# Performance work log

Measured on AMD Instinct MI355X. Metric: run time of the kernel, lower is better.

## Reference

```python
import jax, jax.numpy as jnp
import numpy as np
from itertools import combinations, product

HID = 32
HEADS = 4
HEAD_DIM = 2


def _e8_roots():
    # 240 E8 roots: 112 of form (+-1,+-1,0^6) permuted, 128 of form (+-1/2)^8 with even # of minus signs
    roots = []
    for i, j in combinations(range(8), 2):
        for si in (1.0, -1.0):
            for sj in (1.0, -1.0):
                v = np.zeros(8); v[i] = si; v[j] = sj
                roots.append(v)
    for signs in product((0.5, -0.5), repeat=8):
        if sum(1 for s in signs if s < 0) % 2 == 0:
            roots.append(np.array(signs))
    return jnp.asarray(np.stack(roots), dtype=jnp.float32)  # [240, 8]


def _nearest_d8(x):
    # nearest point of D8 lattice (integer coords, even coordinate sum)
    f = jnp.round(x)
    err = x - f
    idx = jnp.argmax(jnp.abs(err), axis=-1)  # coord with worst rounding error
    oh = jax.nn.one_hot(idx, 8, dtype=x.dtype)
    e_at = jnp.take_along_axis(err, idx[..., None], axis=-1)  # [B,1]
    g = f + oh * jnp.where(e_at >= 0, 1.0, -1.0)  # flip worst coord the other way
    parity_ok = jnp.mod(f.sum(-1), 2.0) == 0
    return jnp.where(parity_ok[..., None], f, g)


def _nearest_e8(x):
    # E8 = D8  U  (D8 + 1/2)
    y0 = _nearest_d8(x)
    y1 = _nearest_d8(x - 0.5) + 0.5
    d0 = ((x - y0) ** 2).sum(-1, keepdims=True)
    d1 = ((x - y1) ** 2).sum(-1, keepdims=True)
    return jnp.where(d0 <= d1, y0, y1)


def _norm(x, eps=1e-12):
    return x / jnp.maximum(jnp.linalg.norm(x, axis=-1, keepdims=True), eps)


def setup_inputs() -> dict:
    key = jax.random.key(0)
    ks = jax.random.split(key, 16)
    B, N = 524288, 7
    s8, s32 = 1.0 / np.sqrt(8.0), 1.0 / np.sqrt(32.0)
    return {
        'colony_outputs': jax.random.normal(ks[0], (B, N, 8), jnp.float32),
        'colony_confidences': jax.random.uniform(ks[1], (B, N), jnp.float32),
        'Wq': jax.random.uniform(ks[2], (HID, 8), jnp.float32, -s8, s8),
        'bq': jnp.zeros((HID,), jnp.float32),
        'Wk': jax.random.uniform(ks[3], (HID, 8), jnp.float32, -s8, s8),
        'bk': jnp.zeros((HID,), jnp.float32),
        'Wv': jax.random.uniform(ks[4], (8, 8), jnp.float32, -s8, s8),
        'bv': jnp.zeros((8,), jnp.float32),
        'comm': jnp.eye(N, dtype=jnp.float32) + 0.1 * jax.random.normal(ks[5], (N, N), jnp.float32),
        'role': jnp.ones((N,), jnp.float32) + 0.1 * jax.random.normal(ks[6], (N,), jnp.float32),
        'mha_in_w': jax.random.uniform(ks[7], (24, 8), jnp.float32, -s8, s8),
        'mha_in_b': jnp.zeros((24,), jnp.float32),
        'W1': jax.random.uniform(ks[8], (HID, 8), jnp.float32, -s8, s8),
        'b1': jnp.zeros((HID,), jnp.float32),
        'W2': jax.random.uniform(ks[9], (8, HID), jnp.float32, -s32, s32),
        'b2': jnp.zeros((8,), jnp.float32),
        'gate': jnp.asarray(0.1, jnp.float32),
    }


def reference(colony_outputs, colony_confidences, Wq, bq, Wk, bk, Wv, bv,
              comm, role, mha_in_w, mha_in_b, W1, b1, W2, b2, gate):
    roots = _e8_roots()  # [240, 8]
    x = _norm(colony_outputs)  # [B, N, 8] on S^7
    B, N, _ = x.shape

    # --- attention-based colony weights ---
    q = x.mean(axis=1) @ Wq.T + bq                 # [B, HID]
    k = x @ Wk.T + bk                              # [B, N, HID]
    scores = jnp.einsum('bh,bnh->bn', q, k) / np.sqrt(float(HID))
    scores = jnp.einsum('bn,nm->bm', scores, jax.nn.softmax(comm, axis=-1))
    scores = scores + jax.nn.softmax(role)[None, :]

    # multi-head attention weights (embed 8, 4 heads, head_dim 2); dropout off (eval)
    Wq3, Wk3 = mha_in_w[:8], mha_in_w[8:16]
    bq3, bk3 = mha_in_b[:8], mha_in_b[8:16]
    Q = (x @ Wq3.T + bq3).reshape(B, N, HEADS, HEAD_DIM)
    K = (x @ Wk3.T + bk3).reshape(B, N, HEADS, HEAD_DIM)
    A = jax.nn.softmax(jnp.einsum('bnhd,bmhd->bhnm', Q, K) / np.sqrt(float(HEAD_DIM)), axis=-1)
    mhs = A.mean(axis=1).mean(axis=1)              # avg heads -> [B,N,N], mean over queries -> [B,N]
    scores = 0.7 * scores + 0.3 * mhs
    weights = jax.nn.softmax(scores, axis=-1)      # [B, N]

    # confidence modulation
    weights = weights * colony_confidences
    weights = weights / jnp.clip(weights.sum(-1, keepdims=True), 1e-8, None)

    # combine + gated MLP refine
    values = x @ Wv.T + bv                         # [B, N, 8]
    combined = jnp.einsum('bn,bnd->bd', weights, values)  # [B, 8]
    h = jax.nn.gelu(combined @ W1.T + b1, approximate=False) @ W2.T + b2
    refined = _norm(combined + jax.nn.sigmoid(gate) * h)

    # E8 quantization with straight-through estimator (training path)
    hard = _nearest_e8(refined)
    quantized = refined + jax.lax.stop_gradient(hard - refined)
    sq = (refined ** 2).sum(-1, keepdims=True) - 2.0 * refined @ roots.T + (roots ** 2).sum(-1)[None, :]
    indices = jnp.argmin(sq, axis=-1)              # [B]
    return quantized, indices, weights
```

## Files before the change

### kernel.cpp

```cpp
#include <hip/hip_runtime.h>
#include <math.h>

#define INV_SQRT2 0.70710678118654752f
#define INV_SQRT32 0.17677669529663689f

__device__ __forceinline__ void nearest_d8(const float* xx, float* y) {
  float f[8], err[8];
#pragma unroll
  for (int d = 0; d < 8; ++d) { f[d] = rintf(xx[d]); err[d] = xx[d] - f[d]; }
  int idx = 0; float best = -1.0f;
#pragma unroll
  for (int d = 0; d < 8; ++d) { float a = fabsf(err[d]); if (a > best) { best = a; idx = d; } }
  float fs = 0.f;
#pragma unroll
  for (int d = 0; d < 8; ++d) fs += f[d];
  bool ok = ((((int)fs) & 1) == 0);
#pragma unroll
  for (int d = 0; d < 8; ++d) {
    float g = f[d] + ((d == idx) ? ((err[d] >= 0.f) ? 1.f : -1.f) : 0.f);
    y[d] = ok ? f[d] : g;
  }
}

__device__ __forceinline__ float pair_sum(float mine, int half) {
  float o = __shfl_xor(mine, 1, 64);
  return half ? (o + mine) : (mine + o);
}

extern "C" __global__ void __launch_bounds__(256)
e8_kernel(const float* __restrict__ colony, const float* __restrict__ conf,
          const float* __restrict__ Wq, const float* __restrict__ bq,
          const float* __restrict__ Wk, const float* __restrict__ bk,
          const float* __restrict__ Wv, const float* __restrict__ bv,
          const float* __restrict__ comm, const float* __restrict__ role,
          const float* __restrict__ mha_w, const float* __restrict__ mha_b,
          const float* __restrict__ W1, const float* __restrict__ b1,
          const float* __restrict__ W2, const float* __restrict__ b2,
          const float* __restrict__ gate, float* __restrict__ out, int B)
{
  __shared__ float x_lds[56 * 128];
  __shared__ float wlds[7 * 128];
  __shared__ float sM8[64], sU[8], sV[8], sCc[1];
  __shared__ float sComm[49], sRole[7];
  __shared__ float sWq3[64], sWk3[64], sBq3[8], sBk3[8];
  __shared__ float sWv[64], sBv[8];
  __shared__ float sW1[256], sB1[32], sW2[256], sB2[8];
  __shared__ float sGate[1];

  const int t = threadIdx.x;
  if (t < 64) {
    int i = t >> 3, j = t & 7;
    float a = 0.f;
    for (int h = 0; h < 32; ++h) a += Wq[h * 8 + i] * Wk[h * 8 + j];
    sM8[t] = a;
    sWq3[t] = mha_w[t];
    sWk3[t] = mha_w[64 + t];
    sWv[t] = Wv[t];
  } else if (t < 72) {
    int j = t - 64;
    float a = 0.f, bb = 0.f;
    for (int h = 0; h < 32; ++h) { a += bq[h] * Wk[h * 8 + j]; bb += bk[h] * Wq[h * 8 + j]; }
    sU[j] = a; sV[j] = bb;
    sBq3[j] = mha_b[j]; sBk3[j] = mha_b[8 + j]; sBv[j] = bv[j]; sB2[j] = b2[j];
  } else if (t == 72) {
    float c = 0.f;
    for (int h = 0; h < 32; ++h) c += bq[h] * bk[h];
    sCc[0] = c;
    sGate[0] = 1.f / (1.f + expf(-gate[0]));
  } else if (t >= 80 && t < 87) {
    int n = t - 80;
    float mx = -1e30f;
    for (int m = 0; m < 7; ++m) mx = fmaxf(mx, comm[n * 7 + m]);
    float ee[7], s = 0.f;
    for (int m = 0; m < 7; ++m) { ee[m] = expf(comm[n * 7 + m] - mx); s += ee[m]; }
    for (int m = 0; m < 7; ++m) sComm[n * 7 + m] = ee[m] / s;
  } else if (t == 87) {
    float mx = -1e30f;
    for (int m = 0; m < 7; ++m) mx = fmaxf(mx, role[m]);
    float ee[7], s = 0.f;
    for (int m = 0; m < 7; ++m) { ee[m] = expf(role[m] - mx); s += ee[m]; }
    for (int m = 0; m < 7; ++m) sRole[m] = ee[m] / s;
  }
  sW1[t] = W1[t];
  sW2[t] = W2[t];
  if (t < 32) sB1[t] = b1[t];

  const int eloc = t >> 1;
  const int half = t & 1;
  const int el = blockIdx.x * 128 + eloc;
  const int ec = (el < B) ? el : (B - 1);

  {
    const float* px = colony + (size_t)ec * 56;
#pragma unroll
    for (int nn = 0; nn < 4; ++nn) {
      int n = half * 4 + nn;
      if (n < 7) {
        float4 v0 = *(const float4*)(px + n * 8);
        float4 v1 = *(const float4*)(px + n * 8 + 4);
        float row[8] = { v0.x, v0.y, v0.z, v0.w, v1.x, v1.y, v1.z, v1.w };
        float ss = 0.f;
#pragma unroll
        for (int d = 0; d < 8; ++d) ss += row[d] * row[d];
        float inv = 1.0f / fmaxf(sqrtf(ss), 1e-12f);
#pragma unroll
        for (int d = 0; d < 8; ++d) x_lds[(n * 8 + d) * 128 + eloc] = row[d] * inv;
      }
    }
  }
  __syncthreads();

#define LDX(n, j) x_lds[(((n) << 3) + (j)) * 128 + eloc]

  float xm[8];
#pragma unroll
  for (int d = 0; d < 8; ++d) xm[d] = 0.f;
#pragma unroll
  for (int n = 0; n < 7; ++n) {
#pragma unroll
    for (int d = 0; d < 8; ++d) xm[d] += LDX(n, d);
  }
#pragma unroll
  for (int d = 0; d < 8; ++d) xm[d] *= (1.0f / 7.0f);

  float w8[8];
#pragma unroll
  for (int j = 0; j < 8; ++j) {
    float a = 0.f;
#pragma unroll
    for (int i = 0; i < 8; ++i) a += xm[i] * sM8[i * 8 + j];
    w8[j] = a + sU[j];
  }
  float base = sCc[0];
#pragma unroll
  for (int i = 0; i < 8; ++i) base += sV[i] * xm[i];
  float sc[7];
#pragma unroll
  for (int n = 0; n < 7; ++n) {
    float a = base;
#pragma unroll
    for (int j = 0; j < 8; ++j) a += w8[j] * LDX(n, j);
    sc[n] = a * INV_SQRT32;
  }
  float sc2[7];
#pragma unroll
  for (int m = 0; m < 7; ++m) {
    float a = 0.f;
#pragma unroll
    for (int n = 0; n < 7; ++n) a += sc[n] * sComm[n * 7 + m];
    sc2[m] = a + sRole[m];
  }

  float mhs_p[7];
#pragma unroll
  for (int m = 0; m < 7; ++m) mhs_p[m] = 0.f;
#pragma unroll
  for (int hh = 0; hh < 2; ++hh) {
    int h = half * 2 + hh;
    float Kh[7][2], Qh[7][2];
#pragma unroll
    for (int m = 0; m < 7; ++m) {
      float row[8];
#pragma unroll
      for (int j = 0; j < 8; ++j) row[j] = LDX(m, j);
      float k0 = sBk3[2 * h], k1 = sBk3[2 * h + 1];
      float q0 = sBq3[2 * h], q1 = sBq3[2 * h + 1];
#pragma unroll
      for (int j = 0; j < 8; ++j) {
        k0 += row[j] * sWk3[(2 * h) * 8 + j];
        k1 += row[j] * sWk3[(2 * h + 1) * 8 + j];
        q0 += row[j] * sWq3[(2 * h) * 8 + j];
        q1 += row[j] * sWq3[(2 * h + 1) * 8 + j];
      }
      Kh[m][0] = k0; Kh[m][1] = k1;
      Qh[m][0] = q0; Qh[m][1] = q1;
    }
#pragma unroll
    for (int n = 0; n < 7; ++n) {
      float ex[7], mx = -1e30f;
#pragma unroll
      for (int m = 0; m < 7; ++m) {
        float a = Qh[n][0] * Kh[m][0] + Qh[n][1] * Kh[m][1];
        ex[m] = a * INV_SQRT2;
        mx = fmaxf(mx, ex[m]);
      }
      float s = 0.f;
#pragma unroll
      for (int m = 0; m < 7; ++m) { ex[m] = __expf(ex[m] - mx); s += ex[m]; }
      float inv = 1.0f / s;
#pragma unroll
      for (int m = 0; m < 7; ++m) mhs_p[m] += ex[m] * inv;
    }
  }
  float mhs[7];
#pragma unroll
  for (int m = 0; m < 7; ++m) mhs[m] = pair_sum(mhs_p[m], half);

  float scf[7], mx2 = -1e30f;
#pragma unroll
  for (int m = 0; m < 7; ++m) {
    scf[m] = 0.7f * sc2[m] + 0.3f * ((mhs[m] * 0.25f) * (1.0f / 7.0f));
    mx2 = fmaxf(mx2, scf[m]);
  }
  float ew[7], s2 = 0.f;
#pragma unroll
  for (int m = 0; m < 7; ++m) { ew[m] = __expf(scf[m] - mx2); s2 += ew[m]; }
  float sinv = 1.0f / s2;
  float w[7], ws = 0.f;
  const float* pc = conf + (size_t)ec * 7;
#pragma unroll
  for (int m = 0; m < 7; ++m) { w[m] = (ew[m] * sinv) * pc[m]; ws += w[m]; }
  float dinv = 1.0f / fmaxf(ws, 1e-8f);
#pragma unroll
  for (int m = 0; m < 7; ++m) w[m] = w[m] * dinv;

  if (!half) {
#pragma unroll
    for (int m = 0; m < 7; ++m) wlds[eloc * 7 + m] = w[m];
  }

  float xc[8];
#pragma unroll
  for (int d = 0; d < 8; ++d) xc[d] = 0.f;
#pragma unroll
  for (int n = 0; n < 7; ++n) {
#pragma unroll
    for (int d = 0; d < 8; ++d) xc[d] += w[n] * LDX(n, d);
  }
  float comb[8];
#pragma unroll
  for (int i = 0; i < 8; ++i) {
    float a = sBv[i];
#pragma unroll
    for (int j = 0; j < 8; ++j) a += sWv[i * 8 + j] * xc[j];
    comb[i] = a;
  }

  float o8p[8];
#pragma unroll
  for (int k = 0; k < 8; ++k) o8p[k] = half ? 0.f : sB2[k];
#pragma unroll
  for (int ii = 0; ii < 16; ++ii) {
    int i = half * 16 + ii;
    float a = sB1[i];
#pragma unroll
    for (int j = 0; j < 8; ++j) a += sW1[i * 8 + j] * comb[j];
    float g = 0.5f * a * (1.f + erff(a * INV_SQRT2));
#pragma unroll
    for (int k = 0; k < 8; ++k) o8p[k] += sW2[k * 32 + i] * g;
  }
  float o8[8];
#pragma unroll
  for (int k = 0; k < 8; ++k) o8[k] = pair_sum(o8p[k], half);

  float gsig = sGate[0];
  float pre[8], ss2 = 0.f;
#pragma unroll
  for (int d = 0; d < 8; ++d) { pre[d] = comb[d] + gsig * o8[d]; ss2 += pre[d] * pre[d]; }
  float ninv = 1.0f / fmaxf(sqrtf(ss2), 1e-12f);
  float r[8];
#pragma unroll
  for (int d = 0; d < 8; ++d) r[d] = pre[d] * ninv;

  float* outq = out;
  float* outi = out + (size_t)B * 8;
  float* outw = out + (size_t)B * 9;

  {
    float xs[8], y[8];
#pragma unroll
    for (int d = 0; d < 8; ++d) xs[d] = half ? (r[d] - 0.5f) : r[d];
    nearest_d8(xs, y);
#pragma unroll
    for (int d = 0; d < 8; ++d) y[d] = half ? (y[d] + 0.5f) : y[d];
    float dow = 0.f;
#pragma unroll
    for (int d = 0; d < 8; ++d) { float dd = r[d] - y[d]; dow += dd * dd; }
    float doth = __shfl_xor(dow, 1, 64);
    float dd0 = half ? doth : dow;
    float dd1 = half ? dow : doth;
    bool use0 = (dd0 <= dd1);
    bool mine_wins = (use0 == (half == 0));
    if (mine_wins && el < B) {
      float q0v[8];
#pragma unroll
      for (int d = 0; d < 8; ++d) q0v[d] = r[d] + (y[d] - r[d]);
      *(float4*)(outq + (size_t)el * 8)     = make_float4(q0v[0], q0v[1], q0v[2], q0v[3]);
      *(float4*)(outq + (size_t)el * 8 + 4) = make_float4(q0v[4], q0v[5], q0v[6], q0v[7]);
    }
  }

  float ssum = 0.f;
#pragma unroll
  for (int d = 0; d < 8; ++d) ssum += r[d] * r[d];
  float bestSq = 1e30f;
  int bestIdx = 0;
  {
    int idx = 0;
#pragma unroll
    for (int i = 0; i < 8; ++i) {
#pragma unroll
      for (int j = i + 1; j < 8; ++j) {
        float a = r[i] + r[j];
        float bb = r[i] - r[j];
        float c0 = half ? -bb : a;
        float c1 = half ? -a : bb;
        float sq0 = fmaf(-2.f, c0, ssum) + 2.f;
        if (sq0 < bestSq) { bestSq = sq0; bestIdx = idx + 2 * half; }
        float sq1 = fmaf(-2.f, c1, ssum) + 2.f;
        if (sq1 < bestSq) { bestSq = sq1; bestIdx = idx + 2 * half + 1; }
        idx += 4;
      }
    }
  }
  {
    float hr[8];
#pragma unroll
    for (int d = 0; d < 8; ++d) hr[d] = 0.5f * r[d];
    float sumhr = ((hr[0] + hr[1]) + (hr[2] + hr[3])) + ((hr[4] + hr[5]) + (hr[6] + hr[7]));
    float Thi[16], Tlo[16];
#pragma unroll
    for (int m = 0; m < 16; ++m) {
      float s1 = 0.f, sB_ = 0.f;
      if (m & 8) { s1 += hr[0]; sB_ += hr[4]; }
      if (m & 4) { s1 += hr[1]; sB_ += hr[5]; }
      if (m & 2) { s1 += hr[2]; sB_ += hr[6]; }
      if (m & 1) { s1 += hr[3]; sB_ += hr[7]; }
      Thi[m] = s1; Tlo[m] = sB_;
    }
#pragma unroll
    for (int k = 0; k < 128; ++k) {
      const int c = (k << 1) | (__popc(k) & 1);
      float T = Thi[c >> 4] + Tlo[c & 15];
      float dot = sumhr - 2.f * T;
      float sq = fmaf(-2.f, dot, ssum) + 2.f;
      if (sq < bestSq) { bestSq = sq; bestIdx = 112 + k; }
    }
  }
  {
    float oSq = __shfl_xor(bestSq, 1, 64);
    int oIdx = __shfl_xor(bestIdx, 1, 64);
    if (oSq < bestSq || (oSq == bestSq && oIdx < bestIdx)) { bestSq = oSq; bestIdx = oIdx; }
    if (!half && el < B) outi[el] = (float)bestIdx;
  }

  __syncthreads();
  {
    const size_t wbase = (size_t)blockIdx.x * 896;
    const size_t wtot = (size_t)B * 7;
    float* dst = outw + wbase;
#pragma unroll
    for (int k = 0; k < 4; ++k) {
      int idx = k * 256 + t;
      if (idx < 896 && wbase + idx < wtot) dst[idx] = wlds[idx];
    }
  }
#undef LDX
}

extern "C" void kernel_launch(void* const* d_in, const int* in_sizes, int n_in,
                              void* d_out, int out_size, void* d_ws, size_t ws_size,
                              hipStream_t stream) {
  const float* colony = (const float*)d_in[0];
  const float* conf   = (const float*)d_in[1];
  const float* Wq     = (const float*)d_in[2];
  const float* bq     = (const float*)d_in[3];
  const float* Wk     = (const float*)d_in[4];
  const float* bk     = (const float*)d_in[5];
  const float* Wv     = (const float*)d_in[6];
  const float* bv     = (const float*)d_in[7];
  const float* comm   = (const float*)d_in[8];
  const float* role   = (const float*)d_in[9];
  const float* mhaw   = (const float*)d_in[10];
  const float* mhab   = (const float*)d_in[11];
  const float* W1     = (const float*)d_in[12];
  const float* b1     = (const float*)d_in[13];
  const float* W2     = (const float*)d_in[14];
  const float* b2     = (const float*)d_in[15];
  const float* gate   = (const float*)d_in[16];

  int B = in_sizes[0] / 56;
  dim3 grid((B + 127) / 128), block(256);
  hipLaunchKernelGGL(e8_kernel, grid, block, 0, stream,
                     colony, conf, Wq, bq, Wk, bk, Wv, bv, comm, role,
                     mhaw, mhab, W1, b1, W2, b2, gate, (float*)d_out, B);
}
```

Measured before the change: 164.7 us.

## Split each batch element across four threads instead of two

Each batch element is now processed by a quad of threads instead of a pair, and blocks cover 64 elements instead of 128. The per-element matvecs, attention heads, MLP hidden units and root search are partitioned four ways, with results recombined through width-4 shuffles and xor reductions. The LDS row stride is padded to 65 to avoid bank conflicts. This cuts per-thread serial work and register pressure, at the cost of more shuffle traffic, some redundant work, and twice as many blocks each repeating the weight preload.

Result: faster. 148.0 us (-10.1%).

```diff
diff --git a/kernel.cpp b/kernel.cpp
--- a/kernel.cpp
+++ b/kernel.cpp
@@ -22,9 +22,11 @@
   }
 }
 
-__device__ __forceinline__ float pair_sum(float mine, int half) {
-  float o = __shfl_xor(mine, 1, 64);
-  return half ? (o + mine) : (mine + o);
+__device__ __forceinline__ float qsum(float v, int q) {
+  float o1 = __shfl_xor(v, 1, 64);
+  float s1 = (q & 1) ? (o1 + v) : (v + o1);
+  float o2 = __shfl_xor(s1, 2, 64);
+  return (q & 2) ? (o2 + s1) : (s1 + o2);
 }
 
 extern "C" __global__ void __launch_bounds__(256)
@@ -38,8 +40,8 @@
           const float* __restrict__ W2, const float* __restrict__ b2,
           const float* __restrict__ gate, float* __restrict__ out, int B)
 {
-  __shared__ float x_lds[56 * 128];
-  __shared__ float wlds[7 * 128];
+  __shared__ float x_lds[56 * 65];
+  __shared__ float wlds[7 * 64];
   __shared__ float sM8[64], sU[8], sV[8], sCc[1];
   __shared__ float sComm[49], sRole[7];
   __shared__ float sWq3[64], sWk3[64], sBq3[8], sBk3[8];
@@ -85,96 +87,114 @@
   sW2[t] = W2[t];
   if (t < 32) sB1[t] = b1[t];
 
-  const int eloc = t >> 1;
-  const int half = t & 1;
-  const int el = blockIdx.x * 128 + eloc;
-  const int ec = (el < B) ? el : (B - 1);
+  const int q    = t & 3;
+  const int eloc = t >> 2;
+  const int el   = blockIdx.x * 64 + eloc;
+  const int ec   = (el < B) ? el : (B - 1);
+  const bool q3  = (q < 3);
+  const int n1 = q;
+  const int n2 = q3 ? q + 4 : 3;
+
+#define LDX(n, j) x_lds[(((n) << 3) + (j)) * 65 + eloc]
 
   {
     const float* px = colony + (size_t)ec * 56;
 #pragma unroll
-    for (int nn = 0; nn < 4; ++nn) {
-      int n = half * 4 + nn;
-      if (n < 7) {
-        float4 v0 = *(const float4*)(px + n * 8);
-        float4 v1 = *(const float4*)(px + n * 8 + 4);
-        float row[8] = { v0.x, v0.y, v0.z, v0.w, v1.x, v1.y, v1.z, v1.w };
-        float ss = 0.f;
-#pragma unroll
-        for (int d = 0; d < 8; ++d) ss += row[d] * row[d];
-        float inv = 1.0f / fmaxf(sqrtf(ss), 1e-12f);
-#pragma unroll
-        for (int d = 0; d < 8; ++d) x_lds[(n * 8 + d) * 128 + eloc] = row[d] * inv;
-      }
+    for (int rr = 0; rr < 2; ++rr) {
+      int n = rr ? n2 : n1;
+      float4 v0 = *(const float4*)(px + n * 8);
+      float4 v1 = *(const float4*)(px + n * 8 + 4);
+      float row[8] = { v0.x, v0.y, v0.z, v0.w, v1.x, v1.y, v1.z, v1.w };
+      float ss = 0.f;
+#pragma unroll
+      for (int d = 0; d < 8; ++d) ss += row[d] * row[d];
+      float inv = 1.0f / fmaxf(sqrtf(ss), 1e-12f);
+#pragma unroll
+      for (int d = 0; d < 8; ++d) x_lds[((n << 3) + d) * 65 + eloc] = row[d] * inv;
     }
   }
   __syncthreads();
 
-#define LDX(n, j) x_lds[(((n) << 3) + (j)) * 128 + eloc]
-
   float xm[8];
 #pragma unroll
-  for (int d = 0; d < 8; ++d) xm[d] = 0.f;
-#pragma unroll
-  for (int n = 0; n < 7; ++n) {
-#pragma unroll
-    for (int d = 0; d < 8; ++d) xm[d] += LDX(n, d);
-  }
-#pragma unroll
-  for (int d = 0; d < 8; ++d) xm[d] *= (1.0f / 7.0f);
+  for (int d = 0; d < 8; ++d) {
+    float a = LDX(n1, d);
+    float bpart = LDX(n2, d);
+    float p = q3 ? (a + bpart) : a;
+    xm[d] = qsum(p, q) * (1.0f / 7.0f);
+  }
 
   float w8[8];
-#pragma unroll
-  for (int j = 0; j < 8; ++j) {
-    float a = 0.f;
-#pragma unroll
-    for (int i = 0; i < 8; ++i) a += xm[i] * sM8[i * 8 + j];
-    w8[j] = a + sU[j];
+  {
+    float a0 = 0.f, a1 = 0.f;
+#pragma unroll
+    for (int i = 0; i < 8; ++i) {
+      a0 += xm[i] * sM8[i * 8 + q];
+      a1 += xm[i] * sM8[i * 8 + q + 4];
+    }
+    a0 += sU[q]; a1 += sU[q + 4];
+#pragma unroll
+    for (int j = 0; j < 4; ++j) w8[j] = __shfl(a0, j, 4);
+#pragma unroll
+    for (int j = 4; j < 8; ++j) w8[j] = __shfl(a1, j - 4, 4);
   }
   float base = sCc[0];
 #pragma unroll
   for (int i = 0; i < 8; ++i) base += sV[i] * xm[i];
+
   float sc[7];
-#pragma unroll
-  for (int n = 0; n < 7; ++n) {
-    float a = base;
-#pragma unroll
-    for (int j = 0; j < 8; ++j) a += w8[j] * LDX(n, j);
-    sc[n] = a * INV_SQRT32;
-  }
+  {
+    float sA = base, sB_ = base;
+#pragma unroll
+    for (int j = 0; j < 8; ++j) {
+      sA  += w8[j] * LDX(n1, j);
+      sB_ += w8[j] * LDX(n2, j);
+    }
+    sA *= INV_SQRT32; sB_ *= INV_SQRT32;
+#pragma unroll
+    for (int n = 0; n < 4; ++n) sc[n] = __shfl(sA, n, 4);
+#pragma unroll
+    for (int n = 4; n < 7; ++n) sc[n] = __shfl(sB_, n - 4, 4);
+  }
+
   float sc2[7];
-#pragma unroll
-  for (int m = 0; m < 7; ++m) {
-    float a = 0.f;
-#pragma unroll
-    for (int n = 0; n < 7; ++n) a += sc[n] * sComm[n * 7 + m];
-    sc2[m] = a + sRole[m];
-  }
-
-  float mhs_p[7];
-#pragma unroll
-  for (int m = 0; m < 7; ++m) mhs_p[m] = 0.f;
-#pragma unroll
-  for (int hh = 0; hh < 2; ++hh) {
-    int h = half * 2 + hh;
+  {
+    float a0 = 0.f, a1 = 0.f;
+#pragma unroll
+    for (int n = 0; n < 7; ++n) {
+      a0 += sc[n] * sComm[n * 7 + q];
+      a1 += sc[n] * sComm[n * 7 + n2];
+    }
+    a0 += sRole[q]; a1 += sRole[n2];
+#pragma unroll
+    for (int m = 0; m < 4; ++m) sc2[m] = __shfl(a0, m, 4);
+#pragma unroll
+    for (int m = 4; m < 7; ++m) sc2[m] = __shfl(a1, m - 4, 4);
+  }
+
+  float mhs[7];
+  {
     float Kh[7][2], Qh[7][2];
 #pragma unroll
     for (int m = 0; m < 7; ++m) {
       float row[8];
 #pragma unroll
       for (int j = 0; j < 8; ++j) row[j] = LDX(m, j);
-      float k0 = sBk3[2 * h], k1 = sBk3[2 * h + 1];
-      float q0 = sBq3[2 * h], q1 = sBq3[2 * h + 1];
+      float k0 = sBk3[2 * q], k1 = sBk3[2 * q + 1];
+      float q0 = sBq3[2 * q], q1 = sBq3[2 * q + 1];
 #pragma unroll
       for (int j = 0; j < 8; ++j) {
-        k0 += row[j] * sWk3[(2 * h) * 8 + j];
-        k1 += row[j] * sWk3[(2 * h + 1) * 8 + j];
-        q0 += row[j] * sWq3[(2 * h) * 8 + j];
-        q1 += row[j] * sWq3[(2 * h + 1) * 8 + j];
+        k0 += row[j] * sWk3[(2 * q) * 8 + j];
+        k1 += row[j] * sWk3[(2 * q + 1) * 8 + j];
+        q0 += row[j] * sWq3[(2 * q) * 8 + j];
+        q1 += row[j] * sWq3[(2 * q + 1) * 8 + j];
       }
       Kh[m][0] = k0; Kh[m][1] = k1;
       Qh[m][0] = q0; Qh[m][1] = q1;
     }
+    float mp[7];
+#pragma unroll
+    for (int m = 0; m < 7; ++m) mp[m] = 0.f;
 #pragma unroll
     for (int n = 0; n < 7; ++n) {
       float ex[7], mx = -1e30f;
@@ -189,12 +209,11 @@
       for (int m = 0; m < 7; ++m) { ex[m] = __expf(ex[m] - mx); s += ex[m]; }
       float inv = 1.0f / s;
 #pragma unroll
-      for (int m = 0; m < 7; ++m) mhs_p[m] += ex[m] * inv;
-    }
-  }
-  float mhs[7];
-#pragma unroll
-  for (int m = 0; m < 7; ++m) mhs[m] = pair_sum(mhs_p[m], half);
+      for (int m = 0; m < 7; ++m) mp[m] += ex[m] * inv;
+    }
+#pragma unroll
+    for (int m = 0; m < 7; ++m) mhs[m] = qsum(mp[m], q);
+  }
 
   float scf[7], mx2 = -1e30f;
 #pragma unroll
@@ -214,50 +233,63 @@
 #pragma unroll
   for (int m = 0; m < 7; ++m) w[m] = w[m] * dinv;
 
-  if (!half) {
+  if (q == 0) {
 #pragma unroll
     for (int m = 0; m < 7; ++m) wlds[eloc * 7 + m] = w[m];
   }
 
   float xc[8];
-#pragma unroll
-  for (int d = 0; d < 8; ++d) xc[d] = 0.f;
-#pragma unroll
-  for (int n = 0; n < 7; ++n) {
-#pragma unroll
-    for (int d = 0; d < 8; ++d) xc[d] += w[n] * LDX(n, d);
-  }
+  {
+    float a0 = 0.f, a1 = 0.f;
+#pragma unroll
+    for (int n = 0; n < 7; ++n) {
+      a0 += w[n] * LDX(n, q);
+      a1 += w[n] * LDX(n, q + 4);
+    }
+#pragma unroll
+    for (int d = 0; d < 4; ++d) xc[d] = __shfl(a0, d, 4);
+#pragma unroll
+    for (int d = 4; d < 8; ++d) xc[d] = __shfl(a1, d - 4, 4);
+  }
+
   float comb[8];
-#pragma unroll
-  for (int i = 0; i < 8; ++i) {
-    float a = sBv[i];
-#pragma unroll
-    for (int j = 0; j < 8; ++j) a += sWv[i * 8 + j] * xc[j];
-    comb[i] = a;
-  }
-
-  float o8p[8];
-#pragma unroll
-  for (int k = 0; k < 8; ++k) o8p[k] = half ? 0.f : sB2[k];
-#pragma unroll
-  for (int ii = 0; ii < 16; ++ii) {
-    int i = half * 16 + ii;
-    float a = sB1[i];
-#pragma unroll
-    for (int j = 0; j < 8; ++j) a += sW1[i * 8 + j] * comb[j];
-    float g = 0.5f * a * (1.f + erff(a * INV_SQRT2));
-#pragma unroll
-    for (int k = 0; k < 8; ++k) o8p[k] += sW2[k * 32 + i] * g;
-  }
+  {
+    float a0 = sBv[q], a1 = sBv[q + 4];
+#pragma unroll
+    for (int j = 0; j < 8; ++j) {
+      a0 += sWv[q * 8 + j] * xc[j];
+      a1 += sWv[(q + 4) * 8 + j] * xc[j];
+    }
+#pragma unroll
+    for (int i = 0; i < 4; ++i) comb[i] = __shfl(a0, i, 4);
+#pragma unroll
+    for (int i = 4; i < 8; ++i) comb[i] = __shfl(a1, i - 4, 4);
+  }
+
   float o8[8];
-#pragma unroll
-  for (int k = 0; k < 8; ++k) o8[k] = pair_sum(o8p[k], half);
+  {
+    float op[8];
+#pragma unroll
+    for (int k = 0; k < 8; ++k) op[k] = (q == 0) ? sB2[k] : 0.f;
+#pragma unroll
+    for (int ii = 0; ii < 8; ++ii) {
+      int i = 8 * q + ii;
+      float a = sB1[i];
+#pragma unroll
+      for (int j = 0; j < 8; ++j) a += sW1[i * 8 + j] * comb[j];
+      float g = 0.5f * a * (1.f + erff(a * INV_SQRT2));
+#pragma unroll
+      for (int k = 0; k < 8; ++k) op[k] += sW2[k * 32 + i] * g;
+    }
+#pragma unroll
+    for (int k = 0; k < 8; ++k) o8[k] = qsum(op[k], q);
+  }
 
   float gsig = sGate[0];
-  float pre[8], ss2 = 0.f;
-#pragma unroll
-  for (int d = 0; d < 8; ++d) { pre[d] = comb[d] + gsig * o8[d]; ss2 += pre[d] * pre[d]; }
-  float ninv = 1.0f / fmaxf(sqrtf(ss2), 1e-12f);
+  float pre[8], ssq = 0.f;
+#pragma unroll
+  for (int d = 0; d < 8; ++d) { pre[d] = comb[d] + gsig * o8[d]; ssq += pre[d] * pre[d]; }
+  float ninv = 1.0f / fmaxf(sqrtf(ssq), 1e-12f);
   float r[8];
 #pragma unroll
   for (int d = 0; d < 8; ++d) r[d] = pre[d] * ninv;
@@ -267,26 +299,27 @@
   float* outw = out + (size_t)B * 9;
 
   {
+    const int h2 = q >> 1;
     float xs[8], y[8];
 #pragma unroll
-    for (int d = 0; d < 8; ++d) xs[d] = half ? (r[d] - 0.5f) : r[d];
+    for (int d = 0; d < 8; ++d) xs[d] = h2 ? (r[d] - 0.5f) : r[d];
     nearest_d8(xs, y);
 #pragma unroll
-    for (int d = 0; d < 8; ++d) y[d] = half ? (y[d] + 0.5f) : y[d];
+    for (int d = 0; d < 8; ++d) y[d] = h2 ? (y[d] + 0.5f) : y[d];
     float dow = 0.f;
 #pragma unroll
     for (int d = 0; d < 8; ++d) { float dd = r[d] - y[d]; dow += dd * dd; }
-    float doth = __shfl_xor(dow, 1, 64);
-    float dd0 = half ? doth : dow;
-    float dd1 = half ? dow : doth;
+    float doth = __shfl_xor(dow, 2, 64);
+    float dd0 = h2 ? doth : dow;
+    float dd1 = h2 ? dow : doth;
     bool use0 = (dd0 <= dd1);
-    bool mine_wins = (use0 == (half == 0));
-    if (mine_wins && el < B) {
-      float q0v[8];
-#pragma unroll
-      for (int d = 0; d < 8; ++d) q0v[d] = r[d] + (y[d] - r[d]);
-      *(float4*)(outq + (size_t)el * 8)     = make_float4(q0v[0], q0v[1], q0v[2], q0v[3]);
-      *(float4*)(outq + (size_t)el * 8 + 4) = make_float4(q0v[4], q0v[5], q0v[6], q0v[7]);
+    bool mine_wins = (use0 == (h2 == 0));
+    if (mine_wins && ((q & 1) == 0) && el < B) {
+      float qv[8];
+#pragma unroll
+      for (int d = 0; d < 8; ++d) qv[d] = r[d] + (y[d] - r[d]);
+      *(float4*)(outq + (size_t)el * 8)     = make_float4(qv[0], qv[1], qv[2], qv[3]);
+      *(float4*)(outq + (size_t)el * 8 + 4) = make_float4(qv[4], qv[5], qv[6], qv[7]);
     }
   }
 
@@ -303,56 +336,68 @@
       for (int j = i + 1; j < 8; ++j) {
         float a = r[i] + r[j];
         float bb = r[i] - r[j];
-        float c0 = half ? -bb : a;
-        float c1 = half ? -a : bb;
-        float sq0 = fmaf(-2.f, c0, ssum) + 2.f;
-        if (sq0 < bestSq) { bestSq = sq0; bestIdx = idx + 2 * half; }
-        float sq1 = fmaf(-2.f, c1, ssum) + 2.f;
-        if (sq1 < bestSq) { bestSq = sq1; bestIdx = idx + 2 * half + 1; }
+        float t1 = (q & 2) ? -bb : a;
+        float t2 = (q & 2) ? -a  : bb;
+        float c  = (q & 1) ? t2 : t1;
+        float sq = fmaf(-2.f, c, ssum) + 2.f;
+        if (sq < bestSq) { bestSq = sq; bestIdx = idx; }
         idx += 4;
       }
     }
+    bestIdx += q;
   }
   {
     float hr[8];
 #pragma unroll
     for (int d = 0; d < 8; ++d) hr[d] = 0.5f * r[d];
     float sumhr = ((hr[0] + hr[1]) + (hr[2] + hr[3])) + ((hr[4] + hr[5]) + (hr[6] + hr[7]));
-    float Thi[16], Tlo[16];
-#pragma unroll
-    for (int m = 0; m < 16; ++m) {
-      float s1 = 0.f, sB_ = 0.f;
-      if (m & 8) { s1 += hr[0]; sB_ += hr[4]; }
-      if (m & 4) { s1 += hr[1]; sB_ += hr[5]; }
-      if (m & 2) { s1 += hr[2]; sB_ += hr[6]; }
-      if (m & 1) { s1 += hr[3]; sB_ += hr[7]; }
-      Thi[m] = s1; Tlo[m] = sB_;
-    }
-#pragma unroll
-    for (int k = 0; k < 128; ++k) {
-      const int c = (k << 1) | (__popc(k) & 1);
-      float T = Thi[c >> 4] + Tlo[c & 15];
+    float tb0 = (q & 2) ? hr[0] : 0.f;
+    float tb  = (q & 1) ? (tb0 + hr[1]) : tb0;
+    float Th[4];
+    Th[0] = tb;
+    Th[1] = tb + hr[3];
+    Th[2] = tb + hr[2];
+    Th[3] = (tb + hr[2]) + hr[3];
+    float TloB[8];
+    TloB[0] = 0.f;
+    TloB[4] = 0.f + hr[4];
+    TloB[2] = 0.f + hr[5];
+    TloB[6] = hr[4] + hr[5];
+    TloB[1] = 0.f + hr[6];
+    TloB[5] = hr[4] + hr[6];
+    TloB[3] = hr[5] + hr[6];
+    TloB[7] = (hr[4] + hr[5]) + hr[6];
+    const int pq = ((q >> 1) ^ q) & 1;
+    const float hpE = pq ? hr[7] : 0.f;
+    const float hpO = pq ? 0.f : hr[7];
+    const int hbase = 112 + (q << 5);
+#pragma unroll
+    for (int kk = 0; kk < 32; ++kk) {
+      float tl = TloB[kk & 7] + ((__popc(kk) & 1) ? hpO : hpE);
+      float T = Th[kk >> 3] + tl;
       float dot = sumhr - 2.f * T;
       float sq = fmaf(-2.f, dot, ssum) + 2.f;
-      if (sq < bestSq) { bestSq = sq; bestIdx = 112 + k; }
-    }
-  }
-  {
-    float oSq = __shfl_xor(bestSq, 1, 64);
-    int oIdx = __shfl_xor(bestIdx, 1, 64);
-    if (oSq < bestSq || (oSq == bestSq && oIdx < bestIdx)) { bestSq = oSq; bestIdx = oIdx; }
-    if (!half && el < B) outi[el] = (float)bestIdx;
+      if (sq < bestSq) { bestSq = sq; bestIdx = hbase + kk; }
+    }
+  }
+  {
+#pragma unroll
+    for (int mlev = 1; mlev <= 2; mlev <<= 1) {
+      float oSq = __shfl_xor(bestSq, mlev, 64);
+      int   oIx = __shfl_xor(bestIdx, mlev, 64);
+      if (oSq < bestSq || (oSq == bestSq && oIx < bestIdx)) { bestSq = oSq; bestIdx = oIx; }
+    }
+    if (q == 0 && el < B) outi[el] = (float)bestIdx;
   }
 
   __syncthreads();
   {
-    const size_t wbase = (size_t)blockIdx.x * 896;
+    const size_t wbase = (size_t)blockIdx.x * 448;
     const size_t wtot = (size_t)B * 7;
-    float* dst = outw + wbase;
-#pragma unroll
-    for (int k = 0; k < 4; ++k) {
-      int idx = k * 256 + t;
-      if (idx < 896 && wbase + idx < wtot) dst[idx] = wlds[idx];
+#pragma unroll
+    for (int k2 = 0; k2 < 2; ++k2) {
+      int idx2 = k2 * 256 + t;
+      if (idx2 < 448 && wbase + idx2 < wtot) outw[wbase + idx2] = wlds[idx2];
     }
   }
 #undef LDX
@@ -380,7 +425,7 @@
   const float* gate   = (const float*)d_in[16];
 
   int B = in_sizes[0] / 56;
-  dim3 grid((B + 127) / 128), block(256);
+  dim3 grid((B + 63) / 64), block(256);
   hipLaunchKernelGGL(e8_kernel, grid, block, 0, stream,
                      colony, conf, Wq, bq, Wk, bk, Wv, bv, comm, role,
                      mhaw, mhab, W1, b1, W2, b2, gate, (float*)d_out, B);
```
